# Optimization experiments

Measured on AMD Instinct MI355X. Metric: run time of the kernel, lower is better.

The kernel has to match this reference:

```python
import jax, jax.numpy as jnp
import numpy as np

STRIDES = (8, 16, 32)
NUM_CLASSES = 80
BINS = 16
TOPK = 10
W_CLS, W_IOU, W_DFL = 0.5, 7.5, 1.5
EPS = 1e-9


def make_grid(H, W, stride):
    ys, xs = jnp.meshgrid(jnp.arange(H, dtype=jnp.float32),
                          jnp.arange(W, dtype=jnp.float32), indexing='ij')
    return jnp.stack([(xs + 0.5) * stride, (ys + 0.5) * stride], -1).reshape(-1, 2)


def decode_dfl(dfl, grid, stride):
    # dfl: (B, 64, H, W), channel layout coord-major (4 coords x 16 bins)
    B, C, H, W = dfl.shape
    prob = jax.nn.softmax(dfl.reshape(B, 4, BINS, H, W), axis=2)
    proj = jnp.arange(BINS, dtype=dfl.dtype)
    dist = jnp.einsum('bkchw,c->bkhw', prob, proj)              # expected bin value
    dist = dist.transpose(0, 2, 3, 1).reshape(B, H * W, 4) * stride  # (B,N,4) ltrb px
    cx, cy = grid[:, 0], grid[:, 1]
    return jnp.stack([cx - dist[..., 0], cy - dist[..., 1],
                      cx + dist[..., 2], cy + dist[..., 3]], -1)   # (B,N,4) xyxy


def pairwise_iou(gt, pr, eps=1e-7):
    # gt (B,G,4), pr (B,N,4) -> (B,G,N)
    lt = jnp.maximum(gt[:, :, None, :2], pr[:, None, :, :2])
    rb = jnp.minimum(gt[:, :, None, 2:], pr[:, None, :, 2:])
    wh = jnp.clip(rb - lt, 0.0)
    inter = wh[..., 0] * wh[..., 1]
    ag = jnp.clip(gt[..., 2] - gt[..., 0], 0) * jnp.clip(gt[..., 3] - gt[..., 1], 0)
    ap = jnp.clip(pr[..., 2] - pr[..., 0], 0) * jnp.clip(pr[..., 3] - pr[..., 1], 0)
    return inter / (ag[:, :, None] + ap[:, None, :] - inter + eps)


def ciou(b1, b2, eps=1e-7):
    # elementwise CIoU over (...,4) xyxy boxes
    w1, h1 = b1[..., 2] - b1[..., 0], b1[..., 3] - b1[..., 1]
    w2, h2 = b2[..., 2] - b2[..., 0], b2[..., 3] - b2[..., 1]
    lt = jnp.maximum(b1[..., :2], b2[..., :2])
    rb = jnp.minimum(b1[..., 2:], b2[..., 2:])
    wh = jnp.clip(rb - lt, 0.0)
    inter = wh[..., 0] * wh[..., 1]
    union = w1 * h1 + w2 * h2 - inter + eps
    iou = inter / union
    cw = jnp.maximum(b1[..., 2], b2[..., 2]) - jnp.minimum(b1[..., 0], b2[..., 0])
    ch = jnp.maximum(b1[..., 3], b2[..., 3]) - jnp.minimum(b1[..., 1], b2[..., 1])
    c2 = cw * cw + ch * ch + eps
    rho2 = ((b1[..., 0] + b1[..., 2] - b2[..., 0] - b2[..., 2]) ** 2 +
            (b1[..., 1] + b1[..., 3] - b2[..., 1] - b2[..., 3]) ** 2) / 4.0
    v = (4.0 / np.pi ** 2) * (jnp.arctan(w2 / (h2 + eps)) - jnp.arctan(w1 / (h1 + eps))) ** 2
    a = jax.lax.stop_gradient(v / (v - iou + (1.0 + eps)))
    return iou - rho2 / c2 - a * v


def tal_assign(scores, pred_boxes, gt_bboxes, gt_labels, grid, topk=TOPK, alpha=0.5, beta=6.0):
    B, N, C = scores.shape
    G = gt_bboxes.shape[1]
    mask_gt = gt_bboxes.sum(-1) > 0                                    # (B,G) zero-padded gts
    cx, cy = grid[None, None, :, 0], grid[None, None, :, 1]
    in_gts = ((cx > gt_bboxes[..., 0:1]) & (cx < gt_bboxes[..., 2:3]) &
              (cy > gt_bboxes[..., 1:2]) & (cy < gt_bboxes[..., 3:4]))  # (B,G,N)
    iou = pairwise_iou(gt_bboxes, pred_boxes)                          # (B,G,N)
    probs = jax.nn.sigmoid(scores)                                     # (B,N,C)
    idx = jnp.broadcast_to(gt_labels[:, None, :], (B, N, G))
    cls_g = jnp.take_along_axis(probs, idx, axis=2).transpose(0, 2, 1)  # (B,G,N)
    valid = in_gts & mask_gt[:, :, None]
    align = jnp.where(valid, (cls_g ** alpha) * (iou ** beta), 0.0)
    vals, idxk = jax.lax.top_k(align, topk)                            # (B,G,K)
    bi = jnp.arange(B)[:, None, None]
    gi = jnp.arange(G)[None, :, None]
    topk_mask = jnp.zeros((B, G, N), bool).at[bi, gi, idxk].set(vals > EPS)
    mask_pos = topk_mask & valid
    # resolve anchors assigned to multiple gts: keep gt with highest IoU
    multi = mask_pos.sum(1) > 1                                        # (B,N)
    best_gt = jnp.argmax(iou, axis=1)                                  # (B,N)
    best_oh = best_gt[:, None, :] == jnp.arange(G)[None, :, None]      # (B,G,N)
    mask_pos = jnp.where(multi[:, None, :], best_oh, mask_pos)
    fg_mask = mask_pos.any(1)                                          # (B,N)
    matched = jnp.argmax(mask_pos, axis=1)                             # (B,N)
    matched_gt_inds = jnp.where(fg_mask, matched, -1)
    target_bboxes = jnp.take_along_axis(gt_bboxes, matched[:, :, None], axis=1)
    target_labels = jnp.take_along_axis(gt_labels, matched, axis=1)
    t1h = jax.nn.one_hot(target_labels, C, dtype=scores.dtype) * fg_mask[..., None]
    align_pos = align * mask_pos
    pos_align_max = align_pos.max(2, keepdims=True)                    # per-gt max metric
    pos_iou_max = (iou * mask_pos).max(2, keepdims=True)               # per-gt max overlap
    norm = (align_pos * pos_iou_max / (pos_align_max + EPS)).max(1)    # (B,N)
    target_scores = t1h * norm[..., None]
    return target_scores, target_bboxes, fg_mask, matched_gt_inds


def yolo_loss(p0, p1, p2, gt_bboxes, gt_labels):
    scores_l, dfl_l, boxes_l, grids_l = [], [], [], []
    for p, s in zip((p0, p1, p2), STRIDES):
        B, _, H, W = p.shape
        N = H * W
        dfl, cls = p[:, :64], p[:, 64:64 + NUM_CLASSES]
        grid = make_grid(H, W, s)
        boxes_l.append(decode_dfl(dfl, grid, s))
        scores_l.append(cls.transpose(0, 2, 3, 1).reshape(B, N, NUM_CLASSES))
        dfl_l.append(dfl.transpose(0, 2, 3, 1).reshape(B, N, 4, BINS))
        grids_l.append(grid)
    all_scores = jnp.concatenate(scores_l, 1)      # (B,Nt,80)
    all_dfl = jnp.concatenate(dfl_l, 1)            # (B,Nt,4,16)
    pred_boxes = jnp.concatenate(boxes_l, 1)       # (B,Nt,4)
    grid = jnp.concatenate(grids_l, 0)             # (Nt,2)
    t_scores, t_boxes, fg, matched = tal_assign(all_scores, pred_boxes, gt_bboxes, gt_labels, grid)
    fgf = fg.astype(all_scores.dtype)
    num_pos = jnp.maximum(fgf.sum(), 1.0)
    # BCE with logits, stable form, soft targets
    s = all_scores
    bce = jnp.clip(s, 0.0) - s * t_scores + jnp.log1p(jnp.exp(-jnp.abs(s)))
    loss_cls = bce.sum() / num_pos
    loss_iou = ((1.0 - ciou(pred_boxes, t_boxes)) * fgf).sum() / num_pos  # mean over positives
    # DFL soft targets (original calls _make_dfl_targets with stride=1)
    m = jnp.clip(matched, 0)
    boxes = jnp.take_along_axis(gt_bboxes, m[:, :, None], axis=1)         # (B,Nt,4)
    gcx, gcy = grid[None, :, 0], grid[None, :, 1]
    dists = jnp.stack([jnp.clip(gcx - boxes[..., 0], 0.0),
                       jnp.clip(gcy - boxes[..., 1], 0.0),
                       jnp.clip(boxes[..., 2] - gcx, 0.0),
                       jnp.clip(boxes[..., 3] - gcy, 0.0)], -1)           # (B,Nt,4)
    tb = jnp.clip(dists, 0.0, BINS - 1 - 1e-6)
    lo = jnp.floor(tb)
    a = tb - lo
    li = lo.astype(jnp.int32)
    ui = jnp.minimum(li + 1, BINS - 1)
    td = (jax.nn.one_hot(li, BINS, dtype=tb.dtype) * (1.0 - a)[..., None] +
          jax.nn.one_hot(ui, BINS, dtype=tb.dtype) * a[..., None])        # (B,Nt,4,16)
    td = td * fgf[:, :, None, None]
    lsm = jax.nn.log_softmax(all_dfl, axis=-1)
    loss_dfl = -(td * lsm).sum() / num_pos
    return jnp.stack([W_IOU * loss_iou, W_CLS * loss_cls, W_DFL * loss_dfl])


def setup_inputs() -> dict:
    key = jax.random.key(0)
    k = jax.random.split(key, 6)
    B, G = 32, 32
    p0 = jax.random.normal(k[0], (B, 144, 80, 80), jnp.float32)
    p1 = jax.random.normal(k[1], (B, 144, 40, 40), jnp.float32)
    p2 = jax.random.normal(k[2], (B, 144, 20, 20), jnp.float32)
    c = jax.random.uniform(k[3], (B, G, 2), minval=60.0, maxval=580.0)
    wh = jax.random.uniform(k[4], (B, G, 2), minval=20.0, maxval=200.0)
    gt_bboxes = jnp.concatenate([jnp.clip(c - wh / 2, 0.0, 640.0),
                                 jnp.clip(c + wh / 2, 0.0, 640.0)], -1)
    gt_labels = jax.random.randint(k[5], (B, G), 0, NUM_CLASSES)
    return {'p0': p0, 'p1': p1, 'p2': p2, 'gt_bboxes': gt_bboxes, 'gt_labels': gt_labels}


def reference(p0, p1, p2, gt_bboxes, gt_labels):
    return yolo_loss(p0, p1, p2, gt_bboxes, gt_labels)
```

## Files before the change

### kernel.cpp

```cpp
#include <hip/hip_runtime.h>
#include <hip/hip_bf16.h>

#define NB 32
#define NG 32
#define NC 80
#define NBINS 16
#define NTOT 8400
#define CH 144

#define NBLK1 1050
#define NBLKN 33
#define NBLK3 (NBLKN * NB)

struct AInfo {
    const float* base;
    int hw;
    int off;
    float cx, cy, stride;
};

__device__ __forceinline__ AInfo anchor_info(int n, int b, const float* p0, const float* p1, const float* p2) {
    AInfo ai;
    if (n < 6400) {
        int x = n % 80, y = n / 80;
        ai.hw = 6400; ai.off = n;
        ai.cx = (x + 0.5f) * 8.0f; ai.cy = (y + 0.5f) * 8.0f; ai.stride = 8.0f;
        ai.base = p0 + (size_t)b * CH * 6400;
    } else if (n < 8000) {
        int m = n - 6400; int x = m % 40, y = m / 40;
        ai.hw = 1600; ai.off = m;
        ai.cx = (x + 0.5f) * 16.0f; ai.cy = (y + 0.5f) * 16.0f; ai.stride = 16.0f;
        ai.base = p1 + (size_t)b * CH * 1600;
    } else {
        int m = n - 8000; int x = m % 20, y = m / 20;
        ai.hw = 400; ai.off = m;
        ai.cx = (x + 0.5f) * 32.0f; ai.cy = (y + 0.5f) * 32.0f; ai.stride = 32.0f;
        ai.base = p2 + (size_t)b * CH * 400;
    }
    return ai;
}

__device__ __forceinline__ void ins10(float a[10], float v) {
    if (v > a[9]) {
        a[9] = v;
#pragma unroll
        for (int i = 8; i >= 0; i--) {
            if (a[i + 1] > a[i]) { float t = a[i]; a[i] = a[i + 1]; a[i + 1] = t; }
        }
    }
}

__device__ __forceinline__ float iou_fn(float4 gb, float4 pb, float ap) {
    float ag = fmaxf(gb.z - gb.x, 0.f) * fmaxf(gb.w - gb.y, 0.f);
    float iw = fmaxf(fminf(gb.z, pb.z) - fmaxf(gb.x, pb.x), 0.f);
    float ih = fmaxf(fminf(gb.w, pb.w) - fmaxf(gb.y, pb.y), 0.f);
    float inter = iw * ih;
    return inter / (ag + ap - inter + 1e-7f);
}

__device__ __forceinline__ float ciou_fn(float4 p, float4 t) {
    float w1 = p.z - p.x, h1 = p.w - p.y;
    float w2 = t.z - t.x, h2 = t.w - t.y;
    float iw = fmaxf(fminf(p.z, t.z) - fmaxf(p.x, t.x), 0.f);
    float ih = fmaxf(fminf(p.w, t.w) - fmaxf(p.y, t.y), 0.f);
    float inter = iw * ih;
    float un = w1 * h1 + w2 * h2 - inter + 1e-7f;
    float iou = inter / un;
    float cw = fmaxf(p.z, t.z) - fminf(p.x, t.x);
    float chh = fmaxf(p.w, t.w) - fminf(p.y, t.y);
    float c2 = cw * cw + chh * chh + 1e-7f;
    float dx = p.x + p.z - t.x - t.z, dy = p.y + p.w - t.y - t.w;
    float rho2 = (dx * dx + dy * dy) * 0.25f;
    float da = atanf(w2 / (h2 + 1e-7f)) - atanf(w1 / (h1 + 1e-7f));
    float v = 0.4052847345693511f * da * da;
    float al = v / (v - iou + 1.f + 1e-7f);
    return iou - rho2 / c2 - al * v;
}

__global__ void k0_zero(float* posA, float* posI) {
    int t = threadIdx.x;
    for (int i = t; i < NB * NG; i += 256) { posA[i] = 0.f; posI[i] = 0.f; }
}

__global__ __launch_bounds__(256) void k1_decode(
    const float* __restrict__ p0, const float* __restrict__ p1, const float* __restrict__ p2,
    float* __restrict__ pred, float* __restrict__ lse, float* __restrict__ part_bce) {
    int t = blockIdx.x * 256 + threadIdx.x;
    float bce = 0.f;
    {
        int b = t / NTOT, n = t % NTOT;
        AInfo ai = anchor_info(n, b, p0, p1, p2);
        const float* base = ai.base + ai.off;
        float dist[4], lv[4];
#pragma unroll
        for (int k = 0; k < 4; k++) {
            float v[16]; float mx = -1e30f;
#pragma unroll
            for (int j = 0; j < 16; j++) { v[j] = base[(size_t)(k * 16 + j) * ai.hw]; mx = fmaxf(mx, v[j]); }
            float se = 0.f, we = 0.f;
#pragma unroll
            for (int j = 0; j < 16; j++) { float e = __expf(v[j] - mx); se += e; we += e * (float)j; }
            dist[k] = we / se * ai.stride;
            lv[k] = mx + __logf(se);
        }
        float4 pb = { ai.cx - dist[0], ai.cy - dist[1], ai.cx + dist[2], ai.cy + dist[3] };
        ((float4*)pred)[(size_t)b * NTOT + n] = pb;
        float4 l4 = { lv[0], lv[1], lv[2], lv[3] };
        ((float4*)lse)[(size_t)b * NTOT + n] = l4;
#pragma unroll 4
        for (int c = 0; c < NC; c++) {
            float s = base[(size_t)(64 + c) * ai.hw];
            bce += fmaxf(s, 0.f) + __logf(1.f + __expf(-fabsf(s)));
        }
    }
#pragma unroll
    for (int off = 32; off > 0; off >>= 1) bce += __shfl_xor(bce, off, 64);
    __shared__ float red[4];
    if ((threadIdx.x & 63) == 0) red[threadIdx.x >> 6] = bce;
    __syncthreads();
    if (threadIdx.x == 0)
        part_bce[blockIdx.x] = red[0] + red[1] + red[2] + red[3];
}

__global__ __launch_bounds__(256) void k2_align(
    const float* __restrict__ p0, const float* __restrict__ p1, const float* __restrict__ p2,
    const float* __restrict__ gtb, const int* __restrict__ gtl,
    const float* __restrict__ pred, float* __restrict__ alignv, float* __restrict__ thr) {
    int g = blockIdx.x, b = blockIdx.y;
    const float* gb = gtb + (size_t)(b * NG + g) * 4;
    float gx1 = gb[0], gy1 = gb[1], gx2 = gb[2], gy2 = gb[3];
    bool vg = (gx1 + gy1 + gx2 + gy2) > 0.f;
    int label = gtl[b * NG + g];
    float ag = fmaxf(gx2 - gx1, 0.f) * fmaxf(gy2 - gy1, 0.f);
    float top[10];
#pragma unroll
    for (int i = 0; i < 10; i++) top[i] = -1.f;
    for (int n = threadIdx.x; n < NTOT; n += 256) {
        AInfo ai = anchor_info(n, b, p0, p1, p2);
        float s = ai.base[(size_t)(64 + label) * ai.hw + ai.off];
        float4 pb = ((const float4*)pred)[(size_t)b * NTOT + n];
        float ap = fmaxf(pb.z - pb.x, 0.f) * fmaxf(pb.w - pb.y, 0.f);
        float iw = fmaxf(fminf(gx2, pb.z) - fmaxf(gx1, pb.x), 0.f);
        float ih = fmaxf(fminf(gy2, pb.w) - fmaxf(gy1, pb.y), 0.f);
        float inter = iw * ih;
        float iou = inter / (ag + ap - inter + 1e-7f);
        bool ing = (ai.cx > gx1) && (ai.cx < gx2) && (ai.cy > gy1) && (ai.cy < gy2);
        float al = 0.f;
        if (ing && vg) {
            float sg = 1.f / (1.f + __expf(-s));
            float i2 = iou * iou;
            al = sqrtf(sg) * i2 * i2 * i2;
        }
        alignv[(size_t)(b * NG + g) * NTOT + n] = al;
        ins10(top, al);
    }
    __shared__ float s_top[256 * 10];
#pragma unroll
    for (int i = 0; i < 10; i++) s_top[threadIdx.x * 10 + i] = top[i];
    __syncthreads();
    if (threadIdx.x < 64) {
        float mt[10];
#pragma unroll
        for (int i = 0; i < 10; i++) mt[i] = -1.f;
        for (int src = threadIdx.x; src < 256; src += 64)
#pragma unroll
            for (int i = 0; i < 10; i++) ins10(mt, s_top[src * 10 + i]);
        float thrv = 0.f;
        for (int r = 0; r < 10; r++) {
            unsigned long long key = ((unsigned long long)__float_as_uint(mt[0]) << 32) | (unsigned)threadIdx.x;
#pragma unroll
            for (int off = 32; off > 0; off >>= 1) {
                unsigned long long o = __shfl_xor(key, off, 64);
                if (o > key) key = o;
            }
            thrv = __uint_as_float((unsigned)(key >> 32));
            if ((key & 63ULL) == (unsigned long long)threadIdx.x) {
#pragma unroll
                for (int i = 0; i < 9; i++) mt[i] = mt[i + 1];
                mt[9] = -1.f;
            }
        }
        if (threadIdx.x == 0) thr[b * NG + g] = thrv;
    }
}

__global__ __launch_bounds__(256) void k3_mask(
    const float* __restrict__ alignv, const float* __restrict__ thr,
    const float* __restrict__ pred, const float* __restrict__ gtb,
    unsigned* __restrict__ maskv, int* __restrict__ matchedv,
    float* __restrict__ posA, float* __restrict__ posI, unsigned* __restrict__ partN) {
    int b = blockIdx.y;
    int n = blockIdx.x * 256 + threadIdx.x;
    __shared__ float s_thr[NG];
    __shared__ float4 s_gt[NG];
    if (threadIdx.x < NG) {
        s_thr[threadIdx.x] = thr[b * NG + threadIdx.x];
        s_gt[threadIdx.x] = ((const float4*)gtb)[b * NG + threadIdx.x];
    }
    __syncthreads();
    bool fg = false;
    if (n < NTOT) {
        unsigned m = 0;
#pragma unroll
        for (int g = 0; g < NG; g++) {
            float a = alignv[(size_t)(b * NG + g) * NTOT + n];
            if (a >= s_thr[g] && a > 1e-9f) m |= (1u << g);
        }
        int cnt = __popc(m);
        int matched = -1;
        if (cnt > 0) {
            float4 pb = ((const float4*)pred)[(size_t)b * NTOT + n];
            float ap = fmaxf(pb.z - pb.x, 0.f) * fmaxf(pb.w - pb.y, 0.f);
            if (cnt > 1) {
                float best = -1.f; int bg = 0;
                for (int g = 0; g < NG; g++) {
                    float iou = iou_fn(s_gt[g], pb, ap);
                    if (iou > best) { best = iou; bg = g; }
                }
                m = 1u << bg;
            }
            for (int g = 0; g < NG; g++) {
                if ((m >> g) & 1u) {
                    float iou = iou_fn(s_gt[g], pb, ap);
                    float a = alignv[(size_t)(b * NG + g) * NTOT + n];
                    atomicMax((int*)&posI[b * NG + g], __float_as_int(iou));
                    atomicMax((int*)&posA[b * NG + g], __float_as_int(a));
                }
            }
            matched = __ffs(m) - 1;
            fg = true;
        }
        maskv[(size_t)b * NTOT + n] = m;
        matchedv[(size_t)b * NTOT + n] = matched;
    }
    unsigned long long bal = __ballot(fg);
    __shared__ unsigned redN[4];
    if ((threadIdx.x & 63) == 0) redN[threadIdx.x >> 6] = (unsigned)__popcll(bal);
    __syncthreads();
    if (threadIdx.x == 0)
        partN[blockIdx.y * gridDim.x + blockIdx.x] = redN[0] + redN[1] + redN[2] + redN[3];
}

__global__ __launch_bounds__(256) void k5_loss(
    const float* __restrict__ p0, const float* __restrict__ p1, const float* __restrict__ p2,
    const float* __restrict__ alignv, const unsigned* __restrict__ maskv, const int* __restrict__ matchedv,
    const float* __restrict__ posA, const float* __restrict__ posI,
    const float* __restrict__ gtb, const int* __restrict__ gtl,
    const float* __restrict__ pred, const float* __restrict__ lse,
    float* __restrict__ part_corr, float* __restrict__ part_liou, float* __restrict__ part_ldfl) {
    int b = blockIdx.y;
    int n = blockIdx.x * 256 + threadIdx.x;
    __shared__ float4 s_gt[NG];
    __shared__ int s_lab[NG];
    __shared__ float s_pa[NG], s_pi[NG];
    if (threadIdx.x < NG) {
        s_gt[threadIdx.x] = ((const float4*)gtb)[b * NG + threadIdx.x];
        s_lab[threadIdx.x] = gtl[b * NG + threadIdx.x];
        s_pa[threadIdx.x] = posA[b * NG + threadIdx.x];
        s_pi[threadIdx.x] = posI[b * NG + threadIdx.x];
    }
    __syncthreads();
    float corr = 0.f, liou = 0.f, ldfl = 0.f;
    if (n < NTOT) {
        int mt = matchedv[(size_t)b * NTOT + n];
        if (mt >= 0) {
            unsigned m = maskv[(size_t)b * NTOT + n];
            float nrm = 0.f;
            for (int g = 0; g < NG; g++) {
                if ((m >> g) & 1u) {
                    float a = alignv[(size_t)(b * NG + g) * NTOT + n];
                    nrm = fmaxf(nrm, a * s_pi[g] / (s_pa[g] + 1e-9f));
                }
            }
            AInfo ai = anchor_info(n, b, p0, p1, p2);
            const float* base = ai.base + ai.off;
            float s = base[(size_t)(64 + s_lab[mt]) * ai.hw];
            corr = s * nrm;
            float4 pb = ((const float4*)pred)[(size_t)b * NTOT + n];
            float4 tb = s_gt[mt];
            liou = 1.f - ciou_fn(pb, tb);
            float4 l4 = ((const float4*)lse)[(size_t)b * NTOT + n];
            float lv[4] = { l4.x, l4.y, l4.z, l4.w };
            float d[4] = { fmaxf(ai.cx - tb.x, 0.f), fmaxf(ai.cy - tb.y, 0.f),
                           fmaxf(tb.z - ai.cx, 0.f), fmaxf(tb.w - ai.cy, 0.f) };
#pragma unroll
            for (int k = 0; k < 4; k++) {
                float tbk = fminf(d[k], 14.999999f);
                float lo = floorf(tbk);
                float afr = tbk - lo;
                int li = (int)lo;
                int ui = min(li + 1, 15);
                float Ll = base[(size_t)(k * 16 + li) * ai.hw];
                float Lu = base[(size_t)(k * 16 + ui) * ai.hw];
                ldfl += lv[k] - ((1.f - afr) * Ll + afr * Lu);
            }
        }
    }
#pragma unroll
    for (int off = 32; off > 0; off >>= 1) {
        corr += __shfl_xor(corr, off, 64);
        liou += __shfl_xor(liou, off, 64);
        ldfl += __shfl_xor(ldfl, off, 64);
    }
    __shared__ float rc[4], ri[4], rd[4];
    if ((threadIdx.x & 63) == 0) {
        int w = threadIdx.x >> 6;
        rc[w] = corr; ri[w] = liou; rd[w] = ldfl;
    }
    __syncthreads();
    if (threadIdx.x == 0) {
        int blk = blockIdx.y * gridDim.x + blockIdx.x;
        part_corr[blk] = rc[0] + rc[1] + rc[2] + rc[3];
        part_liou[blk] = ri[0] + ri[1] + ri[2] + ri[3];
        part_ldfl[blk] = rd[0] + rd[1] + rd[2] + rd[3];
    }
}

__global__ __launch_bounds__(256) void k6_final(
    const float* __restrict__ part_bce, const float* __restrict__ part_corr,
    const float* __restrict__ part_liou, const float* __restrict__ part_ldfl,
    const unsigned* __restrict__ partN, float* __restrict__ out) {
    double bce = 0.0, corr = 0.0, liou = 0.0, ldfl = 0.0, np = 0.0;
    for (int i = threadIdx.x; i < NBLK1; i += 256) bce += (double)part_bce[i];
    for (int i = threadIdx.x; i < NBLK3; i += 256) {
        corr += (double)part_corr[i];
        liou += (double)part_liou[i];
        ldfl += (double)part_ldfl[i];
        np   += (double)partN[i];
    }
#pragma unroll
    for (int off = 32; off > 0; off >>= 1) {
        bce  += __shfl_xor(bce, off, 64);
        corr += __shfl_xor(corr, off, 64);
        liou += __shfl_xor(liou, off, 64);
        ldfl += __shfl_xor(ldfl, off, 64);
        np   += __shfl_xor(np, off, 64);
    }
    __shared__ double rb[4], rc[4], ri[4], rd[4], rn[4];
    if ((threadIdx.x & 63) == 0) {
        int w = threadIdx.x >> 6;
        rb[w] = bce; rc[w] = corr; ri[w] = liou; rd[w] = ldfl; rn[w] = np;
    }
    __syncthreads();
    if (threadIdx.x == 0) {
        bce  = rb[0] + rb[1] + rb[2] + rb[3];
        corr = rc[0] + rc[1] + rc[2] + rc[3];
        liou = ri[0] + ri[1] + ri[2] + ri[3];
        ldfl = rd[0] + rd[1] + rd[2] + rd[3];
        np   = rn[0] + rn[1] + rn[2] + rn[3];
        if (np < 1.0) np = 1.0;
        out[0] = (float)(7.5 * liou / np);
        out[1] = (float)(0.5 * (bce - corr) / np);
        out[2] = (float)(1.5 * ldfl / np);
    }
}

extern "C" void kernel_launch(void* const* d_in, const int* in_sizes, int n_in,
                              void* d_out, int out_size, void* d_ws, size_t ws_size,
                              hipStream_t stream) {
    const float* p0 = (const float*)d_in[0];
    const float* p1 = (const float*)d_in[1];
    const float* p2 = (const float*)d_in[2];
    const float* gtb = (const float*)d_in[3];
    const int* gtl = (const int*)d_in[4];
    float* out = (float*)d_out;

    char* w = (char*)d_ws;
    const size_t BN = (size_t)NB * NTOT;
    float* pred = (float*)w;
    float* lse = pred + BN * 4;
    float* alignv = lse + BN * 4;
    float* thr = alignv + (size_t)NB * NG * NTOT;
    float* posA = thr + NB * NG;
    float* posI = posA + NB * NG;
    unsigned* maskv = (unsigned*)(posI + NB * NG);
    int* matchedv = (int*)(maskv + BN);
    float* part_bce = (float*)(matchedv + BN);
    float* part_corr = part_bce + NBLK1;
    float* part_liou = part_corr + NBLK3;
    float* part_ldfl = part_liou + NBLK3;
    unsigned* partN = (unsigned*)(part_ldfl + NBLK3);

    hipLaunchKernelGGL(k0_zero, dim3(1), dim3(256), 0, stream, posA, posI);
    hipLaunchKernelGGL(k1_decode, dim3(NBLK1), dim3(256), 0, stream,
                       p0, p1, p2, pred, lse, part_bce);
    hipLaunchKernelGGL(k2_align, dim3(NG, NB), dim3(256), 0, stream,
                       p0, p1, p2, gtb, gtl, pred, alignv, thr);
    hipLaunchKernelGGL(k3_mask, dim3(NBLKN, NB), dim3(256), 0, stream,
                       alignv, thr, pred, gtb, maskv, matchedv, posA, posI, partN);
    hipLaunchKernelGGL(k5_loss, dim3(NBLKN, NB), dim3(256), 0, stream,
                       p0, p1, p2, alignv, maskv, matchedv, posA, posI, gtb, gtl, pred, lse,
                       part_corr, part_liou, part_ldfl);
    hipLaunchKernelGGL(k6_final, dim3(1), dim3(256), 0, stream,
                       part_bce, part_corr, part_liou, part_ldfl, partN, out);
}
```

Before: 264.6 us.

## Split decode kernel into per-coordinate DFL decode and vectorized BCE kernel

The fused decode kernel, which had one thread per anchor doing four softmaxes and an 80-class BCE loop, is split in two. The first kernel runs one thread per anchor coordinate for the DFL softmax. The second kernel streams the class logits with float4 loads, one thread per four elements, and writes 21000 partial sums. This raises parallelism and load width on a memory-bound stage, at the cost of an extra launch, a larger partial reduction in the final kernel, and scalar strided stores for pred and lse.

```diff
diff --git a/kernel.cpp b/kernel.cpp
--- a/kernel.cpp
+++ b/kernel.cpp
@@ -8,7 +8,9 @@
 #define NTOT 8400
 #define CH 144
 
-#define NBLK1 1050
+#define BN (NB * NTOT)
+#define NBLK1A ((BN * 4) / 256)
+#define NBLK1B 21000
 #define NBLKN 33
 #define NBLK3 (NBLKN * NB)
 
@@ -82,36 +84,50 @@
     for (int i = t; i < NB * NG; i += 256) { posA[i] = 0.f; posI[i] = 0.f; }
 }
 
-__global__ __launch_bounds__(256) void k1_decode(
+__global__ __launch_bounds__(256) void k1a_decode(
     const float* __restrict__ p0, const float* __restrict__ p1, const float* __restrict__ p2,
-    float* __restrict__ pred, float* __restrict__ lse, float* __restrict__ part_bce) {
-    int t = blockIdx.x * 256 + threadIdx.x;
+    float* __restrict__ pred, float* __restrict__ lse) {
+    int tid = blockIdx.x * 256 + threadIdx.x;
+    int a = tid >> 2;
+    int k = tid & 3;
+    int b = a / NTOT, n = a % NTOT;
+    AInfo ai = anchor_info(n, b, p0, p1, p2);
+    const float* base = ai.base + ai.off + (size_t)(k * 16) * ai.hw;
+    float v[16]; float mx = -1e30f;
+#pragma unroll
+    for (int j = 0; j < 16; j++) { v[j] = base[(size_t)j * ai.hw]; mx = fmaxf(mx, v[j]); }
+    float se = 0.f, we = 0.f;
+#pragma unroll
+    for (int j = 0; j < 16; j++) { float e = __expf(v[j] - mx); se += e; we += e * (float)j; }
+    float dist = we / se * ai.stride;
+    float lv = mx + __logf(se);
+    float c = (k & 1) ? ai.cy : ai.cx;
+    pred[(size_t)a * 4 + k] = (k < 2) ? (c - dist) : (c + dist);
+    lse[(size_t)a * 4 + k] = lv;
+}
+
+__global__ __launch_bounds__(256) void k1b_bce(
+    const float* __restrict__ p0, const float* __restrict__ p1, const float* __restrict__ p2,
+    float* __restrict__ part_bce) {
+    const int E0 = 4096000, E1 = 1024000;
+    int i = blockIdx.x * 256 + threadIdx.x;
+    const float* p; int hw4, li;
+    if (i < E0) { p = p0; hw4 = 1600; li = i; }
+    else if (i < E0 + E1) { p = p1; hw4 = 400; li = i - E0; }
+    else { p = p2; hw4 = 100; li = i - E0 - E1; }
+    int per_b = 80 * hw4;
+    int b = li / per_b;
+    int r = li - b * per_b;
+    int c = r / hw4;
+    int o = r - c * hw4;
+    const float4* src = (const float4*)(p + (size_t)b * CH * (hw4 * 4) + (size_t)(64 + c) * (hw4 * 4));
+    float4 s4 = src[o];
     float bce = 0.f;
     {
-        int b = t / NTOT, n = t % NTOT;
-        AInfo ai = anchor_info(n, b, p0, p1, p2);
-        const float* base = ai.base + ai.off;
-        float dist[4], lv[4];
-#pragma unroll
-        for (int k = 0; k < 4; k++) {
-            float v[16]; float mx = -1e30f;
-#pragma unroll
-            for (int j = 0; j < 16; j++) { v[j] = base[(size_t)(k * 16 + j) * ai.hw]; mx = fmaxf(mx, v[j]); }
-            float se = 0.f, we = 0.f;
-#pragma unroll
-            for (int j = 0; j < 16; j++) { float e = __expf(v[j] - mx); se += e; we += e * (float)j; }
-            dist[k] = we / se * ai.stride;
-            lv[k] = mx + __logf(se);
-        }
-        float4 pb = { ai.cx - dist[0], ai.cy - dist[1], ai.cx + dist[2], ai.cy + dist[3] };
-        ((float4*)pred)[(size_t)b * NTOT + n] = pb;
-        float4 l4 = { lv[0], lv[1], lv[2], lv[3] };
-        ((float4*)lse)[(size_t)b * NTOT + n] = l4;
-#pragma unroll 4
-        for (int c = 0; c < NC; c++) {
-            float s = base[(size_t)(64 + c) * ai.hw];
-            bce += fmaxf(s, 0.f) + __logf(1.f + __expf(-fabsf(s)));
-        }
+        float s = s4.x; bce += fmaxf(s, 0.f) + __logf(1.f + __expf(-fabsf(s)));
+        s = s4.y; bce += fmaxf(s, 0.f) + __logf(1.f + __expf(-fabsf(s)));
+        s = s4.z; bce += fmaxf(s, 0.f) + __logf(1.f + __expf(-fabsf(s)));
+        s = s4.w; bce += fmaxf(s, 0.f) + __logf(1.f + __expf(-fabsf(s)));
     }
 #pragma unroll
     for (int off = 32; off > 0; off >>= 1) bce += __shfl_xor(bce, off, 64);
@@ -321,7 +337,7 @@
     const float* __restrict__ part_liou, const float* __restrict__ part_ldfl,
     const unsigned* __restrict__ partN, float* __restrict__ out) {
     double bce = 0.0, corr = 0.0, liou = 0.0, ldfl = 0.0, np = 0.0;
-    for (int i = threadIdx.x; i < NBLK1; i += 256) bce += (double)part_bce[i];
+    for (int i = threadIdx.x; i < NBLK1B; i += 256) bce += (double)part_bce[i];
     for (int i = threadIdx.x; i < NBLK3; i += 256) {
         corr += (double)part_corr[i];
         liou += (double)part_liou[i];
@@ -366,24 +382,25 @@
     float* out = (float*)d_out;
 
     char* w = (char*)d_ws;
-    const size_t BN = (size_t)NB * NTOT;
     float* pred = (float*)w;
-    float* lse = pred + BN * 4;
-    float* alignv = lse + BN * 4;
+    float* lse = pred + (size_t)BN * 4;
+    float* alignv = lse + (size_t)BN * 4;
     float* thr = alignv + (size_t)NB * NG * NTOT;
     float* posA = thr + NB * NG;
     float* posI = posA + NB * NG;
     unsigned* maskv = (unsigned*)(posI + NB * NG);
     int* matchedv = (int*)(maskv + BN);
     float* part_bce = (float*)(matchedv + BN);
-    float* part_corr = part_bce + NBLK1;
+    float* part_corr = part_bce + NBLK1B;
     float* part_liou = part_corr + NBLK3;
     float* part_ldfl = part_liou + NBLK3;
     unsigned* partN = (unsigned*)(part_ldfl + NBLK3);
 
     hipLaunchKernelGGL(k0_zero, dim3(1), dim3(256), 0, stream, posA, posI);
-    hipLaunchKernelGGL(k1_decode, dim3(NBLK1), dim3(256), 0, stream,
-                       p0, p1, p2, pred, lse, part_bce);
+    hipLaunchKernelGGL(k1a_decode, dim3(NBLK1A), dim3(256), 0, stream,
+                       p0, p1, p2, pred, lse);
+    hipLaunchKernelGGL(k1b_bce, dim3(NBLK1B), dim3(256), 0, stream,
+                       p0, p1, p2, part_bce);
     hipLaunchKernelGGL(k2_align, dim3(NG, NB), dim3(256), 0, stream,
                        p0, p1, p2, gtb, gtl, pred, alignv, thr);
     hipLaunchKernelGGL(k3_mask, dim3(NBLKN, NB), dim3(256), 0, stream,
```

Result: slower. 274.0 us (+3.6%).

## Recompute align metric instead of materializing it, and re-tile decode over anchors

Applied to the files above, without the earlier changes.

Removes the B*G*N alignv buffer. k3_mask and k5_loss now recompute IoU and the align metric per anchor/GT pair, and the label score is loaded only for anchors that lie inside a GT. The decode kernel is re-tiled so four threads share one anchor's DFL coordinates and the class BCE is split across warps. Zeroing of posA/posI is folded into that kernel, removing a separate launch. This trades about 34MB of global writes and reads for extra ALU work and scattered class-score loads.

```diff
diff --git a/kernel.cpp b/kernel.cpp
--- a/kernel.cpp
+++ b/kernel.cpp
@@ -4,11 +4,12 @@
 #define NB 32
 #define NG 32
 #define NC 80
-#define NBINS 16
 #define NTOT 8400
 #define CH 144
-
-#define NBLK1 1050
+#define BN (NB * NTOT)
+
+#define TILES_PER_B 132
+#define NBLK1 (NB * TILES_PER_B)
 #define NBLKN 33
 #define NBLK3 (NBLKN * NB)
 
@@ -58,6 +59,12 @@
     return inter / (ag + ap - inter + 1e-7f);
 }
 
+__device__ __forceinline__ float align_metric(float s, float iou) {
+    float sg = 1.f / (1.f + __expf(-s));
+    float i2 = iou * iou;
+    return sqrtf(sg) * i2 * i2 * i2;
+}
+
 __device__ __forceinline__ float ciou_fn(float4 p, float4 t) {
     float w1 = p.z - p.x, h1 = p.w - p.y;
     float w2 = t.z - t.x, h2 = t.w - t.y;
@@ -77,39 +84,49 @@
     return iou - rho2 / c2 - al * v;
 }
 
-__global__ void k0_zero(float* posA, float* posI) {
-    int t = threadIdx.x;
-    for (int i = t; i < NB * NG; i += 256) { posA[i] = 0.f; posI[i] = 0.f; }
-}
-
-__global__ __launch_bounds__(256) void k1_decode(
+__global__ __launch_bounds__(256) void k1_fused(
     const float* __restrict__ p0, const float* __restrict__ p1, const float* __restrict__ p2,
-    float* __restrict__ pred, float* __restrict__ lse, float* __restrict__ part_bce) {
-    int t = blockIdx.x * 256 + threadIdx.x;
+    float* __restrict__ pred, float* __restrict__ lse, float* __restrict__ part_bce,
+    float* __restrict__ posA, float* __restrict__ posI) {
+    int blk = blockIdx.x;
+    if (blk == 0) {
+        for (int i = threadIdx.x; i < NB * NG; i += 256) { posA[i] = 0.f; posI[i] = 0.f; }
+    }
+    int b = blk / TILES_PER_B;
+    int tile = blk - b * TILES_PER_B;
+    const float* base; int hw, o0, lvl_off, W; float spx;
+    if (tile < 100)      { base = p0; hw = 6400; o0 = tile * 64;          lvl_off = 0;    W = 80; spx = 8.f;  }
+    else if (tile < 125) { base = p1; hw = 1600; o0 = (tile - 100) * 64;  lvl_off = 6400; W = 40; spx = 16.f; }
+    else                 { base = p2; hw = 400;  o0 = (tile - 125) * 64;  lvl_off = 8000; W = 20; spx = 32.f; }
+    base += (size_t)b * CH * hw;
+    int valid = min(64, hw - o0);
+
+    int a = threadIdx.x >> 2, k = threadIdx.x & 3;
+    if (a < valid) {
+        const float* col = base + (size_t)(k * 16) * hw + o0 + a;
+        float v[16]; float mx = -1e30f;
+#pragma unroll
+        for (int j = 0; j < 16; j++) { v[j] = col[(size_t)j * hw]; mx = fmaxf(mx, v[j]); }
+        float se = 0.f, we = 0.f;
+#pragma unroll
+        for (int j = 0; j < 16; j++) { float e = __expf(v[j] - mx); se += e; we += e * (float)j; }
+        float dist = we / se * spx;
+        float lv = mx + __logf(se);
+        int nl = o0 + a;
+        int x = nl % W, y = nl / W;
+        float cx = (x + 0.5f) * spx, cy = (y + 0.5f) * spx;
+        float c = (k & 1) ? cy : cx;
+        size_t ai = (size_t)b * NTOT + lvl_off + nl;
+        pred[ai * 4 + k] = (k < 2) ? (c - dist) : (c + dist);
+        lse[ai * 4 + k] = lv;
+    }
+
+    int wv = threadIdx.x >> 6, ln = threadIdx.x & 63;
     float bce = 0.f;
-    {
-        int b = t / NTOT, n = t % NTOT;
-        AInfo ai = anchor_info(n, b, p0, p1, p2);
-        const float* base = ai.base + ai.off;
-        float dist[4], lv[4];
-#pragma unroll
-        for (int k = 0; k < 4; k++) {
-            float v[16]; float mx = -1e30f;
-#pragma unroll
-            for (int j = 0; j < 16; j++) { v[j] = base[(size_t)(k * 16 + j) * ai.hw]; mx = fmaxf(mx, v[j]); }
-            float se = 0.f, we = 0.f;
-#pragma unroll
-            for (int j = 0; j < 16; j++) { float e = __expf(v[j] - mx); se += e; we += e * (float)j; }
-            dist[k] = we / se * ai.stride;
-            lv[k] = mx + __logf(se);
-        }
-        float4 pb = { ai.cx - dist[0], ai.cy - dist[1], ai.cx + dist[2], ai.cy + dist[3] };
-        ((float4*)pred)[(size_t)b * NTOT + n] = pb;
-        float4 l4 = { lv[0], lv[1], lv[2], lv[3] };
-        ((float4*)lse)[(size_t)b * NTOT + n] = l4;
-#pragma unroll 4
-        for (int c = 0; c < NC; c++) {
-            float s = base[(size_t)(64 + c) * ai.hw];
+    if (ln < valid) {
+        const float* cls = base + (size_t)64 * hw + o0 + ln;
+        for (int c = wv; c < NC; c += 4) {
+            float s = cls[(size_t)c * hw];
             bce += fmaxf(s, 0.f) + __logf(1.f + __expf(-fabsf(s)));
         }
     }
@@ -119,39 +136,33 @@
     if ((threadIdx.x & 63) == 0) red[threadIdx.x >> 6] = bce;
     __syncthreads();
     if (threadIdx.x == 0)
-        part_bce[blockIdx.x] = red[0] + red[1] + red[2] + red[3];
-}
-
-__global__ __launch_bounds__(256) void k2_align(
+        part_bce[blk] = red[0] + red[1] + red[2] + red[3];
+}
+
+__global__ __launch_bounds__(256) void k2_thr(
     const float* __restrict__ p0, const float* __restrict__ p1, const float* __restrict__ p2,
     const float* __restrict__ gtb, const int* __restrict__ gtl,
-    const float* __restrict__ pred, float* __restrict__ alignv, float* __restrict__ thr) {
+    const float* __restrict__ pred, float* __restrict__ thr) {
     int g = blockIdx.x, b = blockIdx.y;
     const float* gb = gtb + (size_t)(b * NG + g) * 4;
     float gx1 = gb[0], gy1 = gb[1], gx2 = gb[2], gy2 = gb[3];
     bool vg = (gx1 + gy1 + gx2 + gy2) > 0.f;
     int label = gtl[b * NG + g];
-    float ag = fmaxf(gx2 - gx1, 0.f) * fmaxf(gy2 - gy1, 0.f);
+    float4 gb4 = { gx1, gy1, gx2, gy2 };
     float top[10];
 #pragma unroll
     for (int i = 0; i < 10; i++) top[i] = -1.f;
     for (int n = threadIdx.x; n < NTOT; n += 256) {
         AInfo ai = anchor_info(n, b, p0, p1, p2);
-        float s = ai.base[(size_t)(64 + label) * ai.hw + ai.off];
         float4 pb = ((const float4*)pred)[(size_t)b * NTOT + n];
         float ap = fmaxf(pb.z - pb.x, 0.f) * fmaxf(pb.w - pb.y, 0.f);
-        float iw = fmaxf(fminf(gx2, pb.z) - fmaxf(gx1, pb.x), 0.f);
-        float ih = fmaxf(fminf(gy2, pb.w) - fmaxf(gy1, pb.y), 0.f);
-        float inter = iw * ih;
-        float iou = inter / (ag + ap - inter + 1e-7f);
+        float iou = iou_fn(gb4, pb, ap);
         bool ing = (ai.cx > gx1) && (ai.cx < gx2) && (ai.cy > gy1) && (ai.cy < gy2);
         float al = 0.f;
         if (ing && vg) {
-            float sg = 1.f / (1.f + __expf(-s));
-            float i2 = iou * iou;
-            al = sqrtf(sg) * i2 * i2 * i2;
-        }
-        alignv[(size_t)(b * NG + g) * NTOT + n] = al;
+            float s = ai.base[(size_t)(64 + label) * ai.hw + ai.off];
+            al = align_metric(s, iou);
+        }
         ins10(top, al);
     }
     __shared__ float s_top[256 * 10];
@@ -185,32 +196,44 @@
 }
 
 __global__ __launch_bounds__(256) void k3_mask(
-    const float* __restrict__ alignv, const float* __restrict__ thr,
-    const float* __restrict__ pred, const float* __restrict__ gtb,
+    const float* __restrict__ p0, const float* __restrict__ p1, const float* __restrict__ p2,
+    const float* __restrict__ thr, const float* __restrict__ pred,
+    const float* __restrict__ gtb, const int* __restrict__ gtl,
     unsigned* __restrict__ maskv, int* __restrict__ matchedv,
     float* __restrict__ posA, float* __restrict__ posI, unsigned* __restrict__ partN) {
     int b = blockIdx.y;
     int n = blockIdx.x * 256 + threadIdx.x;
     __shared__ float s_thr[NG];
     __shared__ float4 s_gt[NG];
+    __shared__ int s_lab[NG];
     if (threadIdx.x < NG) {
         s_thr[threadIdx.x] = thr[b * NG + threadIdx.x];
         s_gt[threadIdx.x] = ((const float4*)gtb)[b * NG + threadIdx.x];
+        s_lab[threadIdx.x] = gtl[b * NG + threadIdx.x];
     }
     __syncthreads();
     bool fg = false;
     if (n < NTOT) {
+        AInfo ai = anchor_info(n, b, p0, p1, p2);
+        float4 pb = ((const float4*)pred)[(size_t)b * NTOT + n];
+        float ap = fmaxf(pb.z - pb.x, 0.f) * fmaxf(pb.w - pb.y, 0.f);
         unsigned m = 0;
-#pragma unroll
+#pragma unroll 4
         for (int g = 0; g < NG; g++) {
-            float a = alignv[(size_t)(b * NG + g) * NTOT + n];
-            if (a >= s_thr[g] && a > 1e-9f) m |= (1u << g);
+            float4 gb4 = s_gt[g];
+            bool vg = (gb4.x + gb4.y + gb4.z + gb4.w) > 0.f;
+            float iou = iou_fn(gb4, pb, ap);
+            bool ing = (ai.cx > gb4.x) && (ai.cx < gb4.z) && (ai.cy > gb4.y) && (ai.cy < gb4.w);
+            float al = 0.f;
+            if (ing && vg) {
+                float s = ai.base[(size_t)(64 + s_lab[g]) * ai.hw + ai.off];
+                al = align_metric(s, iou);
+            }
+            if (al >= s_thr[g] && al > 1e-9f) m |= (1u << g);
         }
         int cnt = __popc(m);
         int matched = -1;
         if (cnt > 0) {
-            float4 pb = ((const float4*)pred)[(size_t)b * NTOT + n];
-            float ap = fmaxf(pb.z - pb.x, 0.f) * fmaxf(pb.w - pb.y, 0.f);
             if (cnt > 1) {
                 float best = -1.f; int bg = 0;
                 for (int g = 0; g < NG; g++) {
@@ -221,10 +244,17 @@
             }
             for (int g = 0; g < NG; g++) {
                 if ((m >> g) & 1u) {
-                    float iou = iou_fn(s_gt[g], pb, ap);
-                    float a = alignv[(size_t)(b * NG + g) * NTOT + n];
+                    float4 gb4 = s_gt[g];
+                    bool vg = (gb4.x + gb4.y + gb4.z + gb4.w) > 0.f;
+                    float iou = iou_fn(gb4, pb, ap);
+                    bool ing = (ai.cx > gb4.x) && (ai.cx < gb4.z) && (ai.cy > gb4.y) && (ai.cy < gb4.w);
+                    float al = 0.f;
+                    if (ing && vg) {
+                        float s = ai.base[(size_t)(64 + s_lab[g]) * ai.hw + ai.off];
+                        al = align_metric(s, iou);
+                    }
                     atomicMax((int*)&posI[b * NG + g], __float_as_int(iou));
-                    atomicMax((int*)&posA[b * NG + g], __float_as_int(a));
+                    atomicMax((int*)&posA[b * NG + g], __float_as_int(al));
                 }
             }
             matched = __ffs(m) - 1;
@@ -243,7 +273,7 @@
 
 __global__ __launch_bounds__(256) void k5_loss(
     const float* __restrict__ p0, const float* __restrict__ p1, const float* __restrict__ p2,
-    const float* __restrict__ alignv, const unsigned* __restrict__ maskv, const int* __restrict__ matchedv,
+    const unsigned* __restrict__ maskv, const int* __restrict__ matchedv,
     const float* __restrict__ posA, const float* __restrict__ posI,
     const float* __restrict__ gtb, const int* __restrict__ gtl,
     const float* __restrict__ pred, const float* __restrict__ lse,
@@ -264,19 +294,28 @@
     if (n < NTOT) {
         int mt = matchedv[(size_t)b * NTOT + n];
         if (mt >= 0) {
+            AInfo ai = anchor_info(n, b, p0, p1, p2);
+            const float* base = ai.base + ai.off;
+            float4 pb = ((const float4*)pred)[(size_t)b * NTOT + n];
+            float ap = fmaxf(pb.z - pb.x, 0.f) * fmaxf(pb.w - pb.y, 0.f);
             unsigned m = maskv[(size_t)b * NTOT + n];
             float nrm = 0.f;
             for (int g = 0; g < NG; g++) {
                 if ((m >> g) & 1u) {
-                    float a = alignv[(size_t)(b * NG + g) * NTOT + n];
-                    nrm = fmaxf(nrm, a * s_pi[g] / (s_pa[g] + 1e-9f));
+                    float4 gb4 = s_gt[g];
+                    bool vg = (gb4.x + gb4.y + gb4.z + gb4.w) > 0.f;
+                    float iou = iou_fn(gb4, pb, ap);
+                    bool ing = (ai.cx > gb4.x) && (ai.cx < gb4.z) && (ai.cy > gb4.y) && (ai.cy < gb4.w);
+                    float al = 0.f;
+                    if (ing && vg) {
+                        float s = base[(size_t)(64 + s_lab[g]) * ai.hw];
+                        al = align_metric(s, iou);
+                    }
+                    nrm = fmaxf(nrm, al * s_pi[g] / (s_pa[g] + 1e-9f));
                 }
             }
-            AInfo ai = anchor_info(n, b, p0, p1, p2);
-            const float* base = ai.base + ai.off;
             float s = base[(size_t)(64 + s_lab[mt]) * ai.hw];
             corr = s * nrm;
-            float4 pb = ((const float4*)pred)[(size_t)b * NTOT + n];
             float4 tb = s_gt[mt];
             liou = 1.f - ciou_fn(pb, tb);
             float4 l4 = ((const float4*)lse)[(size_t)b * NTOT + n];
@@ -366,11 +405,9 @@
     float* out = (float*)d_out;
 
     char* w = (char*)d_ws;
-    const size_t BN = (size_t)NB * NTOT;
     float* pred = (float*)w;
-    float* lse = pred + BN * 4;
-    float* alignv = lse + BN * 4;
-    float* thr = alignv + (size_t)NB * NG * NTOT;
+    float* lse = pred + (size_t)BN * 4;
+    float* thr = lse + (size_t)BN * 4;
     float* posA = thr + NB * NG;
     float* posI = posA + NB * NG;
     unsigned* maskv = (unsigned*)(posI + NB * NG);
@@ -381,15 +418,14 @@
     float* part_ldfl = part_liou + NBLK3;
     unsigned* partN = (unsigned*)(part_ldfl + NBLK3);
 
-    hipLaunchKernelGGL(k0_zero, dim3(1), dim3(256), 0, stream, posA, posI);
-    hipLaunchKernelGGL(k1_decode, dim3(NBLK1), dim3(256), 0, stream,
-                       p0, p1, p2, pred, lse, part_bce);
-    hipLaunchKernelGGL(k2_align, dim3(NG, NB), dim3(256), 0, stream,
-                       p0, p1, p2, gtb, gtl, pred, alignv, thr);
+    hipLaunchKernelGGL(k1_fused, dim3(NBLK1), dim3(256), 0, stream,
+                       p0, p1, p2, pred, lse, part_bce, posA, posI);
+    hipLaunchKernelGGL(k2_thr, dim3(NG, NB), dim3(256), 0, stream,
+                       p0, p1, p2, gtb, gtl, pred, thr);
     hipLaunchKernelGGL(k3_mask, dim3(NBLKN, NB), dim3(256), 0, stream,
-                       alignv, thr, pred, gtb, maskv, matchedv, posA, posI, partN);
+                       p0, p1, p2, thr, pred, gtb, gtl, maskv, matchedv, posA, posI, partN);
     hipLaunchKernelGGL(k5_loss, dim3(NBLKN, NB), dim3(256), 0, stream,
-                       p0, p1, p2, alignv, maskv, matchedv, posA, posI, gtb, gtl, pred, lse,
+                       p0, p1, p2, maskv, matchedv, posA, posI, gtb, gtl, pred, lse,
                        part_corr, part_liou, part_ldfl);
     hipLaunchKernelGGL(k6_final, dim3(1), dim3(256), 0, stream,
                        part_bce, part_corr, part_liou, part_ldfl, partN, out);
```

New measurement: 276.4 us. +4.4%, slower.
